# Optimization experiments

Measured on AMD Instinct MI355X. Metric: run time of the kernel, lower is better.

The kernel has to match this reference:

```python
import jax, jax.numpy as jnp
import numpy as np

NUM_QUANTIZERS = 4  # num_quantizers


def setup_inputs() -> dict:
    key = jax.random.key(0)
    k1, k2 = jax.random.split(key)
    x = jax.random.normal(k1, (8, 64, 128, 128), dtype=jnp.float32)
    codebook = jax.random.normal(k2, (512, 64), dtype=jnp.float32)
    return {"x": x, "codebook": codebook}


def reference(x, codebook):
    """Residual VQ with shared Euclidean codebook, straight-through estimator.

    x: [B, C, H, W] image feature map; codebook: [K, C].
    Returns (quantized [B,C,H,W], indices [B,H,W,Q] int32, commit_loss [Q]).
    """
    B, C, H, W = x.shape
    flat = x.transpose(0, 2, 3, 1).reshape(-1, C)  # [N, C], N = B*H*W
    c_sq = jnp.sum(codebook * codebook, axis=-1)   # [K]

    residual = flat
    quant_out = jnp.zeros_like(flat)
    idx_list, losses = [], []
    for _ in range(NUM_QUANTIZERS):
        # argmin ||r - c||^2 == argmin (||c||^2 - 2 r.c); ||r||^2 constant per row
        dist = c_sq[None, :] - 2.0 * (residual @ codebook.T)  # [N, K]
        idx = jnp.argmin(dist, axis=-1)                        # [N]
        quant = codebook[idx]                                  # [N, C] gather
        # commitment loss: mse(stop_grad(quant), residual)
        losses.append(jnp.mean(jnp.square(jax.lax.stop_gradient(quant) - residual)))
        # straight-through: gradients flow to residual, not codebook
        quant_st = residual + jax.lax.stop_gradient(quant - residual)
        quant_out = quant_out + quant_st
        residual = residual - jax.lax.stop_gradient(quant)
        idx_list.append(idx)

    quantized = quant_out.reshape(B, H, W, C).transpose(0, 3, 1, 2)
    indices = jnp.stack(idx_list, axis=-1).reshape(B, H, W, NUM_QUANTIZERS)
    commit_loss = jnp.stack(losses)
    return quantized, indices, commit_loss
```

## Files before the change

### kernel.cpp

```cpp
#include <hip/hip_runtime.h>


#define NPTS   131072
#define CH     64
#define KCODE  512
#define NQ     4
#define HW     16384
#define BPTS   64
#define BTHR   256
#define CCH    8
#define NCHK   8

__device__ __forceinline__ void load_lds16(const float* g, float* l) {
    __builtin_amdgcn_global_load_lds(
        (const __attribute__((address_space(1))) void*)g,
        (__attribute__((address_space(3))) void*)l, 16, 0, 0);
}

__global__ void prep_cbS(const float* __restrict__ cb, float* __restrict__ cbS) {
    int g = blockIdx.x * 256 + threadIdx.x;
    int c = g >> 9, pos = g & 511;
    int i = pos >> 7, cg = (pos >> 2) & 31, j = pos & 3;
    int k = cg * 16 + i * 4 + j;
    cbS[g] = cb[k * CH + c];
}

__global__ void prep_csq(const float* __restrict__ cb, float* __restrict__ csq) {
    int k = blockIdx.x * 256 + threadIdx.x;
    if (k < KCODE) {
        const float4* row = (const float4*)(cb + (size_t)k * CH);
        float a0 = 0.f, a1 = 0.f, a2 = 0.f, a3 = 0.f;
#pragma unroll
        for (int j = 0; j < CH / 4; ++j) {
            float4 v = row[j];
            a0 = fmaf(v.x, v.x, a0); a1 = fmaf(v.y, v.y, a1);
            a2 = fmaf(v.z, v.z, a2); a3 = fmaf(v.w, v.w, a3);
        }
        csq[k] = (a0 + a1) + (a2 + a3);
    }
}

__global__ __launch_bounds__(BTHR, 3) void rvq_main(
    const float* __restrict__ x, const float* __restrict__ cb,
    const float* __restrict__ cbS, const float* __restrict__ csq_g,
    float* __restrict__ out_quant, float* __restrict__ out_idx,
    float* __restrict__ out_loss)
{
    __shared__ __align__(16) float s_res[CH * BPTS];
    __shared__ __align__(16) float s_buf[2][CCH * KCODE];
    __shared__ __align__(16) float s_csq[KCODE];
    __shared__ int   s_bidx[BPTS];
    __shared__ int   s_idx4[BPTS * NQ];
    __shared__ float s_ls[4 * BPTS];

    const int tid  = threadIdx.x;
    const int lane = tid & 63;
    const int w    = tid >> 6;
    const int cg   = tid & 31;
    const int pg   = tid >> 5;

    const int n0  = blockIdx.x * BPTS;
    const int b   = n0 >> 14;
    const int hw0 = n0 & (HW - 1);
    const float* xbase = x + (size_t)b * CH * HW + hw0;

#pragma unroll
    for (int r = 0; r < 4; ++r) {
        int off = (w * 4 + r) * 256;
        load_lds16(cbS + off + lane * 4, &s_buf[0][off]);
    }

    for (int j = tid; j < CH * BPTS / 4; j += BTHR) {
        int c = j >> 4, p4 = j & 15;
        *(float4*)&s_res[c * BPTS + p4 * 4] =
            *(const float4*)(xbase + (size_t)c * HW + p4 * 4);
    }
    for (int j = tid; j < KCODE; j += BTHR) s_csq[j] = csq_g[j];
    __syncthreads();

    float lossq[NQ], idxf[NQ];

    for (int q = 0; q < NQ; ++q) {
        float acc[8][16];
        {
            const float4* cq4 = (const float4*)(s_csq + cg * 16);
            float4 c0 = cq4[0], c1 = cq4[1], c2 = cq4[2], c3 = cq4[3];
            float ci[16] = {c0.x, c0.y, c0.z, c0.w, c1.x, c1.y, c1.z, c1.w,
                            c2.x, c2.y, c2.z, c2.w, c3.x, c3.y, c3.z, c3.w};
#pragma unroll
            for (int p = 0; p < 8; ++p)
#pragma unroll
                for (int n = 0; n < 16; ++n) acc[p][n] = -0.5f * ci[n];
        }

        for (int chk = 0; chk < NCHK; ++chk) {
            if (!(q == NQ - 1 && chk == NCHK - 1)) {
                const int nchk = (chk + 1 < NCHK) ? chk + 1 : 0;
                const float* src = cbS + nchk * (CCH * KCODE);
                float* dst = s_buf[(chk + 1) & 1];
#pragma unroll
                for (int r = 0; r < 4; ++r) {
                    int off = (w * 4 + r) * 256;
                    load_lds16(src + off + lane * 4, dst + off);
                }
            }

            const float* bufp = s_buf[chk & 1];
#pragma unroll 2
            for (int c = 0; c < CCH; ++c) {
                const float* ar = &s_res[(chk * CCH + c) * BPTS + pg * 8];
                float4 a0 = *(const float4*)(ar + 0);
                float4 a1 = *(const float4*)(ar + 4);
                float av[8] = {a0.x, a0.y, a0.z, a0.w, a1.x, a1.y, a1.z, a1.w};
                const float* br = &bufp[c * KCODE + cg * 4];
#pragma unroll
                for (int nb = 0; nb < 4; ++nb) {
                    float4 bq = *(const float4*)(br + nb * 128);
#pragma unroll
                    for (int p = 0; p < 8; ++p) {
                        acc[p][nb * 4 + 0] = fmaf(av[p], bq.x, acc[p][nb * 4 + 0]);
                        acc[p][nb * 4 + 1] = fmaf(av[p], bq.y, acc[p][nb * 4 + 1]);
                        acc[p][nb * 4 + 2] = fmaf(av[p], bq.z, acc[p][nb * 4 + 2]);
                        acc[p][nb * 4 + 3] = fmaf(av[p], bq.w, acc[p][nb * 4 + 3]);
                    }
                }
            }
            __syncthreads();
        }

        float bd[8]; int bi[8];
#pragma unroll
        for (int p = 0; p < 8; ++p) {
            float B = acc[p][0]; int I = cg * 16;
#pragma unroll
            for (int n = 1; n < 16; ++n)
                if (acc[p][n] > B) { B = acc[p][n]; I = cg * 16 + n; }
            bd[p] = B; bi[p] = I;
        }

#pragma unroll
        for (int m = 1; m <= 16; m <<= 1) {
#pragma unroll
            for (int p = 0; p < 8; ++p) {
                float oB = __shfl_xor(bd[p], m, 64);
                int   oI = __shfl_xor(bi[p], m, 64);
                if (oB > bd[p] || (oB == bd[p] && oI < bi[p])) {
                    bd[p] = oB; bi[p] = oI;
                }
            }
        }
        if (cg == 0) {
#pragma unroll
            for (int p = 0; p < 8; ++p) {
                s_bidx[pg * 8 + p] = bi[p];
                s_idx4[(pg * 8 + p) * 4 + q] = bi[p];
            }
        }
        __syncthreads();
        if (tid < BPTS) idxf[q] = (float)s_bidx[tid];

        {
            const int p  = tid & 63;
            const int cq = tid >> 6;
            int bix = s_bidx[p];
            const float4* crow = (const float4*)(cb + (size_t)bix * CH + cq * 16);
            float l0 = 0.f, l1 = 0.f, l2 = 0.f, l3 = 0.f;
#pragma unroll
            for (int i = 0; i < 4; ++i) {
                float4 v = crow[i];
                int c = cq * 16 + i * 4;
                float r0 = s_res[(c + 0) * BPTS + p] - v.x;
                float r1 = s_res[(c + 1) * BPTS + p] - v.y;
                float r2 = s_res[(c + 2) * BPTS + p] - v.z;
                float r3 = s_res[(c + 3) * BPTS + p] - v.w;
                s_res[(c + 0) * BPTS + p] = r0;
                s_res[(c + 1) * BPTS + p] = r1;
                s_res[(c + 2) * BPTS + p] = r2;
                s_res[(c + 3) * BPTS + p] = r3;
                l0 = fmaf(r0, r0, l0); l1 = fmaf(r1, r1, l1);
                l2 = fmaf(r2, r2, l2); l3 = fmaf(r3, r3, l3);
            }
            s_ls[cq * BPTS + p] = (l0 + l1) + (l2 + l3);
        }
        __syncthreads();
        if (tid < BPTS)
            lossq[q] = (s_ls[0 * BPTS + tid] + s_ls[1 * BPTS + tid]) +
                       (s_ls[2 * BPTS + tid] + s_ls[3 * BPTS + tid]);
    }

    {
        const int p  = tid & 63;
        const int cq = tid >> 6;
        int e0 = s_idx4[p * 4 + 0], e1 = s_idx4[p * 4 + 1];
        int e2 = s_idx4[p * 4 + 2], e3 = s_idx4[p * 4 + 3];
        const float4* r0 = (const float4*)(cb + (size_t)e0 * CH + cq * 16);
        const float4* r1 = (const float4*)(cb + (size_t)e1 * CH + cq * 16);
        const float4* r2 = (const float4*)(cb + (size_t)e2 * CH + cq * 16);
        const float4* r3 = (const float4*)(cb + (size_t)e3 * CH + cq * 16);
        float* ob = out_quant + (size_t)b * CH * HW + hw0;
#pragma unroll
        for (int i = 0; i < 4; ++i) {
            float4 v0 = r0[i], v1 = r1[i], v2 = r2[i], v3 = r3[i];
            float s0 = ((v0.x + v1.x) + v2.x) + v3.x;
            float s1 = ((v0.y + v1.y) + v2.y) + v3.y;
            float s2 = ((v0.z + v1.z) + v2.z) + v3.z;
            float s3 = ((v0.w + v1.w) + v2.w) + v3.w;
            int c = cq * 16 + i * 4;
            ob[(size_t)(c + 0) * HW + p] = s0;
            ob[(size_t)(c + 1) * HW + p] = s1;
            ob[(size_t)(c + 2) * HW + p] = s2;
            ob[(size_t)(c + 3) * HW + p] = s3;
        }
    }

    if (tid < BPTS) {
        ((float4*)out_idx)[n0 + tid] =
            make_float4(idxf[0], idxf[1], idxf[2], idxf[3]);
#pragma unroll
        for (int qq = 0; qq < NQ; ++qq) {
            float v = lossq[qq];
            for (int off = 32; off > 0; off >>= 1) v += __shfl_down(v, off, 64);
            if (tid == 0)
                atomicAdd(&out_loss[qq], v * (1.0f / 8388608.0f));
        }
    }
}

extern "C" void kernel_launch(void* const* d_in, const int* in_sizes, int n_in,
                              void* d_out, int out_size, void* d_ws, size_t ws_size,
                              hipStream_t stream) {
    const float* x  = (const float*)d_in[0];
    const float* cb = (const float*)d_in[1];
    float* out       = (float*)d_out;
    float* out_quant = out;
    float* out_idx   = out + 8388608;
    float* out_loss  = out + 8388608 + 524288;

    float* cbS = (float*)d_ws;
    float* csq = cbS + CH * KCODE;

    hipMemsetAsync(out_loss, 0, NQ * sizeof(float), stream);
    prep_cbS<<<(CH * KCODE) / 256, 256, 0, stream>>>(cb, cbS);
    prep_csq<<<2, 256, 0, stream>>>(cb, csq);
    rvq_main<<<NPTS / BPTS, BTHR, 0, stream>>>(x, cb, cbS, csq,
                                               out_quant, out_idx, out_loss);
}
```

Measured before the change: 521.8 us.

## Double block threads to 512 and halve per-thread point tile

Each block now runs 512 threads, and each thread accumulates 4 points by 16 codes instead of 8 by 16. The codebook chunk staging, the residual update and the final gather are split across 8 waves instead of 4. The aim is to cut register pressure per thread and raise the number of resident waves to hide LDS and global latency. The cost is lower FMA-to-LDS-load reuse per thread and more threads taking part in each barrier.

```diff
diff --git a/kernel.cpp b/kernel.cpp
--- a/kernel.cpp
+++ b/kernel.cpp
@@ -7,7 +7,7 @@
 #define NQ     4
 #define HW     16384
 #define BPTS   64
-#define BTHR   256
+#define BTHR   512
 #define CCH    8
 #define NCHK   8
 
@@ -40,7 +40,7 @@
     }
 }
 
-__global__ __launch_bounds__(BTHR, 3) void rvq_main(
+__global__ __launch_bounds__(BTHR, 4) void rvq_main(
     const float* __restrict__ x, const float* __restrict__ cb,
     const float* __restrict__ cbS, const float* __restrict__ csq_g,
     float* __restrict__ out_quant, float* __restrict__ out_idx,
@@ -51,7 +51,7 @@
     __shared__ __align__(16) float s_csq[KCODE];
     __shared__ int   s_bidx[BPTS];
     __shared__ int   s_idx4[BPTS * NQ];
-    __shared__ float s_ls[4 * BPTS];
+    __shared__ float s_ls[8 * BPTS];
 
     const int tid  = threadIdx.x;
     const int lane = tid & 63;
@@ -65,8 +65,8 @@
     const float* xbase = x + (size_t)b * CH * HW + hw0;
 
 #pragma unroll
-    for (int r = 0; r < 4; ++r) {
-        int off = (w * 4 + r) * 256;
+    for (int r = 0; r < 2; ++r) {
+        int off = (w * 2 + r) * 256;
         load_lds16(cbS + off + lane * 4, &s_buf[0][off]);
     }
 
@@ -81,14 +81,14 @@
     float lossq[NQ], idxf[NQ];
 
     for (int q = 0; q < NQ; ++q) {
-        float acc[8][16];
+        float acc[4][16];
         {
             const float4* cq4 = (const float4*)(s_csq + cg * 16);
             float4 c0 = cq4[0], c1 = cq4[1], c2 = cq4[2], c3 = cq4[3];
             float ci[16] = {c0.x, c0.y, c0.z, c0.w, c1.x, c1.y, c1.z, c1.w,
                             c2.x, c2.y, c2.z, c2.w, c3.x, c3.y, c3.z, c3.w};
 #pragma unroll
-            for (int p = 0; p < 8; ++p)
+            for (int p = 0; p < 4; ++p)
 #pragma unroll
                 for (int n = 0; n < 16; ++n) acc[p][n] = -0.5f * ci[n];
         }
@@ -99,8 +99,8 @@
                 const float* src = cbS + nchk * (CCH * KCODE);
                 float* dst = s_buf[(chk + 1) & 1];
 #pragma unroll
-                for (int r = 0; r < 4; ++r) {
-                    int off = (w * 4 + r) * 256;
+                for (int r = 0; r < 2; ++r) {
+                    int off = (w * 2 + r) * 256;
                     load_lds16(src + off + lane * 4, dst + off);
                 }
             }
@@ -108,16 +108,15 @@
             const float* bufp = s_buf[chk & 1];
 #pragma unroll 2
             for (int c = 0; c < CCH; ++c) {
-                const float* ar = &s_res[(chk * CCH + c) * BPTS + pg * 8];
-                float4 a0 = *(const float4*)(ar + 0);
-                float4 a1 = *(const float4*)(ar + 4);
-                float av[8] = {a0.x, a0.y, a0.z, a0.w, a1.x, a1.y, a1.z, a1.w};
+                const float* ar = &s_res[(chk * CCH + c) * BPTS + pg * 4];
+                float4 a0 = *(const float4*)ar;
+                float av[4] = {a0.x, a0.y, a0.z, a0.w};
                 const float* br = &bufp[c * KCODE + cg * 4];
 #pragma unroll
                 for (int nb = 0; nb < 4; ++nb) {
                     float4 bq = *(const float4*)(br + nb * 128);
 #pragma unroll
-                    for (int p = 0; p < 8; ++p) {
+                    for (int p = 0; p < 4; ++p) {
                         acc[p][nb * 4 + 0] = fmaf(av[p], bq.x, acc[p][nb * 4 + 0]);
                         acc[p][nb * 4 + 1] = fmaf(av[p], bq.y, acc[p][nb * 4 + 1]);
                         acc[p][nb * 4 + 2] = fmaf(av[p], bq.z, acc[p][nb * 4 + 2]);
@@ -128,9 +127,9 @@
             __syncthreads();
         }
 
-        float bd[8]; int bi[8];
-#pragma unroll
-        for (int p = 0; p < 8; ++p) {
+        float bd[4]; int bi[4];
+#pragma unroll
+        for (int p = 0; p < 4; ++p) {
             float B = acc[p][0]; int I = cg * 16;
 #pragma unroll
             for (int n = 1; n < 16; ++n)
@@ -141,7 +140,7 @@
 #pragma unroll
         for (int m = 1; m <= 16; m <<= 1) {
 #pragma unroll
-            for (int p = 0; p < 8; ++p) {
+            for (int p = 0; p < 4; ++p) {
                 float oB = __shfl_xor(bd[p], m, 64);
                 int   oI = __shfl_xor(bi[p], m, 64);
                 if (oB > bd[p] || (oB == bd[p] && oI < bi[p])) {
@@ -151,9 +150,9 @@
         }
         if (cg == 0) {
 #pragma unroll
-            for (int p = 0; p < 8; ++p) {
-                s_bidx[pg * 8 + p] = bi[p];
-                s_idx4[(pg * 8 + p) * 4 + q] = bi[p];
+            for (int p = 0; p < 4; ++p) {
+                s_bidx[pg * 4 + p] = bi[p];
+                s_idx4[(pg * 4 + p) * 4 + q] = bi[p];
             }
         }
         __syncthreads();
@@ -161,14 +160,14 @@
 
         {
             const int p  = tid & 63;
-            const int cq = tid >> 6;
+            const int c8 = tid >> 6;
             int bix = s_bidx[p];
-            const float4* crow = (const float4*)(cb + (size_t)bix * CH + cq * 16);
+            const float4* crow = (const float4*)(cb + (size_t)bix * CH + c8 * 8);
             float l0 = 0.f, l1 = 0.f, l2 = 0.f, l3 = 0.f;
 #pragma unroll
-            for (int i = 0; i < 4; ++i) {
+            for (int i = 0; i < 2; ++i) {
                 float4 v = crow[i];
-                int c = cq * 16 + i * 4;
+                int c = c8 * 8 + i * 4;
                 float r0 = s_res[(c + 0) * BPTS + p] - v.x;
                 float r1 = s_res[(c + 1) * BPTS + p] - v.y;
                 float r2 = s_res[(c + 2) * BPTS + p] - v.z;
@@ -180,32 +179,34 @@
                 l0 = fmaf(r0, r0, l0); l1 = fmaf(r1, r1, l1);
                 l2 = fmaf(r2, r2, l2); l3 = fmaf(r3, r3, l3);
             }
-            s_ls[cq * BPTS + p] = (l0 + l1) + (l2 + l3);
+            s_ls[c8 * BPTS + p] = (l0 + l1) + (l2 + l3);
         }
         __syncthreads();
         if (tid < BPTS)
-            lossq[q] = (s_ls[0 * BPTS + tid] + s_ls[1 * BPTS + tid]) +
-                       (s_ls[2 * BPTS + tid] + s_ls[3 * BPTS + tid]);
+            lossq[q] = ((s_ls[0 * BPTS + tid] + s_ls[1 * BPTS + tid]) +
+                        (s_ls[2 * BPTS + tid] + s_ls[3 * BPTS + tid])) +
+                       ((s_ls[4 * BPTS + tid] + s_ls[5 * BPTS + tid]) +
+                        (s_ls[6 * BPTS + tid] + s_ls[7 * BPTS + tid]));
     }
 
     {
         const int p  = tid & 63;
-        const int cq = tid >> 6;
+        const int c8 = tid >> 6;
         int e0 = s_idx4[p * 4 + 0], e1 = s_idx4[p * 4 + 1];
         int e2 = s_idx4[p * 4 + 2], e3 = s_idx4[p * 4 + 3];
-        const float4* r0 = (const float4*)(cb + (size_t)e0 * CH + cq * 16);
-        const float4* r1 = (const float4*)(cb + (size_t)e1 * CH + cq * 16);
-        const float4* r2 = (const float4*)(cb + (size_t)e2 * CH + cq * 16);
-        const float4* r3 = (const float4*)(cb + (size_t)e3 * CH + cq * 16);
+        const float4* r0 = (const float4*)(cb + (size_t)e0 * CH + c8 * 8);
+        const float4* r1 = (const float4*)(cb + (size_t)e1 * CH + c8 * 8);
+        const float4* r2 = (const float4*)(cb + (size_t)e2 * CH + c8 * 8);
+        const float4* r3 = (const float4*)(cb + (size_t)e3 * CH + c8 * 8);
         float* ob = out_quant + (size_t)b * CH * HW + hw0;
 #pragma unroll
-        for (int i = 0; i < 4; ++i) {
+        for (int i = 0; i < 2; ++i) {
             float4 v0 = r0[i], v1 = r1[i], v2 = r2[i], v3 = r3[i];
             float s0 = ((v0.x + v1.x) + v2.x) + v3.x;
             float s1 = ((v0.y + v1.y) + v2.y) + v3.y;
             float s2 = ((v0.z + v1.z) + v2.z) + v3.z;
             float s3 = ((v0.w + v1.w) + v2.w) + v3.w;
-            int c = cq * 16 + i * 4;
+            int c = c8 * 8 + i * 4;
             ob[(size_t)(c + 0) * HW + p] = s0;
             ob[(size_t)(c + 1) * HW + p] = s1;
             ob[(size_t)(c + 2) * HW + p] = s2;
```

Result: slower. 581.6 us (+11.5%).
